# Kernel optimization log

Hardware: AMD Instinct MI355X
Metric: run time of the kernel (lower is better)

The kernel has to match this reference:

```python
import jax, jax.numpy as jnp
import numpy as np

B = 32768; NF = 8; E = 16; V = 100000; D = 4
IN = 2 * NF * E          # 256 = id_dims + agn_dims
FCN = [256, 128, 64]
DIMS = [IN] + FCN
EPS = 1e-5               # BatchNorm1d eps


def setup_inputs() -> dict:
    ks = jax.random.split(jax.random.key(0), 64)
    inp = {
        'id_idx': jax.random.randint(ks[0], (B, NF), 0, V),
        'agn_idx': jax.random.randint(ks[1], (B, NF), 0, V),
        'domain_id': jax.random.randint(ks[2], (B,), 0, D),
        'id_tables': jax.random.normal(ks[3], (NF, V, E), dtype=jnp.float32) * 0.01,
        'agn_tables': jax.random.normal(ks[4], (NF, V, E), dtype=jnp.float32) * 0.01,
    }
    k = 5
    for i in range(len(FCN)):
        din, dout = DIMS[i], DIMS[i + 1]
        inp[f'mlp_W{i}'] = jax.random.normal(ks[k], (D, din, dout), dtype=jnp.float32) / np.sqrt(din).astype(np.float32); k += 1
        inp[f'mlp_b{i}'] = jnp.zeros((D, dout), jnp.float32)
        inp[f'bn_g{i}'] = jnp.ones((D, dout), jnp.float32)
        inp[f'bn_b{i}'] = jnp.zeros((D, dout), jnp.float32)
        inp[f'gate_W1_{i}'] = jax.random.normal(ks[k], (D, IN, dout), dtype=jnp.float32) / np.sqrt(IN).astype(np.float32); k += 1
        inp[f'gate_b1_{i}'] = jnp.zeros((D, dout), jnp.float32)
        inp[f'gate_W2_{i}'] = jax.random.normal(ks[k], (D, dout, dout), dtype=jnp.float32) / np.sqrt(dout).astype(np.float32); k += 1
        inp[f'gate_b2_{i}'] = jnp.zeros((D, dout), jnp.float32)
    inp['fin_W'] = jax.random.normal(ks[k], (D, DIMS[-1], 1), dtype=jnp.float32) / np.sqrt(DIMS[-1]).astype(np.float32)
    inp['fin_b'] = jnp.zeros((D, 1), jnp.float32)
    return inp


def _embed(tables, idx):
    # tables [NF,V,E], idx [B,NF] -> [B, NF*E] (per-feature lookup then concat)
    g = tables[jnp.arange(NF)[None, :], idx]            # [B,NF,E]
    return g.reshape(idx.shape[0], NF * E)


def _ppnet(id_tables, agn_tables, mlp_W, mlp_b, bn_g, bn_b, gW1, gb1, gW2, gb2,
           fin_W, fin_b, id_idx, agn_idx, domain_id):
    id_x = _embed(id_tables, id_idx)                    # [B, 128]
    agn_x = _embed(agn_tables, agn_idx)                 # [B, 128]
    # gate_input = cat(id_x, agn_x.detach())
    gate_in = jnp.concatenate([id_x, jax.lax.stop_gradient(agn_x)], axis=1)  # [B, IN]
    h = None
    for i in range(len(FCN)):
        # GateNU: Linear->ReLU->Linear->2*sigmoid, broadcast over D domain towers
        g1 = jax.nn.relu(jnp.einsum('bi,dio->dbo', gate_in, gW1[i]) + gb1[i][:, None, :])
        gate = 2.0 * jax.nn.sigmoid(jnp.einsum('dbo,dop->dbp', g1, gW2[i]) + gb2[i][:, None, :])
        # MLP layer: Linear -> BatchNorm1d (train-mode batch stats) -> ReLU
        if h is None:
            h = jnp.einsum('bi,dio->dbo', gate_in, mlp_W[i]) + mlp_b[i][:, None, :]
        else:
            h = jnp.einsum('dbi,dio->dbo', h, mlp_W[i]) + mlp_b[i][:, None, :]
        mu = h.mean(axis=1, keepdims=True)
        var = h.var(axis=1, keepdims=True)              # biased, matches torch BN training
        h = (h - mu) * jax.lax.rsqrt(var + EPS) * bn_g[i][:, None, :] + bn_b[i][:, None, :]
        h = jax.nn.relu(h)
        h = h * gate
    out = jax.nn.sigmoid(jnp.einsum('dbh,dho->dbo', h, fin_W) + fin_b[:, None, :])  # [D,B,1]
    out = out[:, :, 0]                                  # [D,B]
    # torch.where masked-select chain == gather the row of the assigned domain
    return out[domain_id, jnp.arange(out.shape[1])]     # [B]


def reference(id_idx, agn_idx, domain_id, id_tables, agn_tables,
              mlp_W0, mlp_b0, bn_g0, bn_b0, gate_W1_0, gate_b1_0, gate_W2_0, gate_b2_0,
              mlp_W1, mlp_b1, bn_g1, bn_b1, gate_W1_1, gate_b1_1, gate_W2_1, gate_b2_1,
              mlp_W2, mlp_b2, bn_g2, bn_b2, gate_W1_2, gate_b1_2, gate_W2_2, gate_b2_2,
              fin_W, fin_b):
    mlp_W = [mlp_W0, mlp_W1, mlp_W2]; mlp_b = [mlp_b0, mlp_b1, mlp_b2]
    bn_g = [bn_g0, bn_g1, bn_g2]; bn_b = [bn_b0, bn_b1, bn_b2]
    gW1 = [gate_W1_0, gate_W1_1, gate_W1_2]; gb1 = [gate_b1_0, gate_b1_1, gate_b1_2]
    gW2 = [gate_W2_0, gate_W2_1, gate_W2_2]; gb2 = [gate_b2_0, gate_b2_1, gate_b2_2]
    return _ppnet(id_tables, agn_tables, mlp_W, mlp_b, bn_g, bn_b, gW1, gb1, gW2, gb2,
                  fin_W, fin_b, id_idx, agn_idx, domain_id)
```

## Files before the change

### kernel.cpp

```cpp
#include <hip/hip_runtime.h>


typedef __attribute__((ext_vector_type(8))) short short8;
typedef __attribute__((ext_vector_type(4))) float floatx4;

#define BATCH 32768
#define NDOM 4
#define TM 64

__device__ __forceinline__ unsigned short f2b(float f) {
    unsigned u = __float_as_uint(f);
    u += 0x7fffu + ((u >> 16) & 1u);
    return (unsigned short)(u >> 16);
}
__device__ __forceinline__ float b2f(unsigned short h) {
    return __uint_as_float(((unsigned)h) << 16);
}

struct MatDesc { const float* src; unsigned K, N, pfx, total; };
struct PrepArgs { MatDesc m[9]; float* stats; unsigned statsN; unsigned grand; };

__global__ __launch_bounds__(256) void prep_k(PrepArgs a, unsigned short* __restrict__ wt) {
    unsigned e = blockIdx.x * 256 + threadIdx.x;
    if (e < a.statsN) a.stats[e] = 0.f;
    if (e >= a.grand) return;
    int j = 0;
    while (j < 8 && e >= a.m[j].pfx + a.m[j].total) j++;
    const unsigned K = a.m[j].K, N = a.m[j].N;
    const unsigned local = e - a.m[j].pfx;
    const unsigned kn = K * N;
    const unsigned d = local / kn;
    const unsigned r2 = local - d * kn;
    const unsigned n = r2 / K;
    const unsigned k = r2 - n * K;
    wt[e] = f2b(a.m[j].src[((long long)d * K + k) * N + n]);
}

__global__ __launch_bounds__(256) void embed_k(const int* __restrict__ idi, const int* __restrict__ agi,
                                               const float* __restrict__ idt, const float* __restrict__ agt,
                                               unsigned short* __restrict__ gin) {
    int t = blockIdx.x * 256 + threadIdx.x;
    int b = t >> 4, slot = t & 15;
    int f = slot & 7;
    const int* ip = (slot < 8) ? idi : agi;
    const float* tab = (slot < 8) ? idt : agt;
    int ix = ip[b * 8 + f];
    const float* src = tab + ((long long)f * 100000 + ix) * 16;
    unsigned short tmp[16];
#pragma unroll
    for (int j = 0; j < 16; j++) tmp[j] = f2b(src[j]);
    unsigned short* dst = gin + (long long)b * 256 + slot * 16;
    *(uint4*)dst = *(const uint4*)tmp;
    *(uint4*)(dst + 8) = *(const uint4*)(tmp + 8);
}

template <int N, int KX>
__global__ __launch_bounds__(256, 2) void stats_k(
    const unsigned short* __restrict__ X, int ginMode,
    const unsigned short* __restrict__ Wm,
    float* __restrict__ gsum, float* __restrict__ gssq) {
    constexpr int GX = KX / 8;
    constexpr int NW = N / 4, CT = NW / 16;
    __shared__ __align__(16) unsigned short tA[TM * KX];
    const int t = threadIdx.x;
    const int d = blockIdx.y;
    const int m0 = blockIdx.x * TM;
    const unsigned short* Xp = X + ((long long)(ginMode ? 0 : d * BATCH) + m0) * KX;
#pragma unroll
    for (int r = 0; r < TM * GX / 256; r++) {
        int idx = r * 256 + t;
        int m = idx / GX, j = idx % GX;
        uint4 v = *(const uint4*)(Xp + (long long)m * KX + j * 8);
        *(uint4*)&tA[(m * GX + (j ^ (m & 7))) * 8] = v;
    }
    __syncthreads();
    const int w = t >> 6, lane = t & 63, lrow = lane & 15, lq = lane >> 4;
    const int n0w = w * NW;
    const unsigned short* Wp = Wm + ((long long)d * N + n0w) * KX;
    floatx4 acc[4][CT];
#pragma unroll
    for (int rt = 0; rt < 4; rt++)
#pragma unroll
        for (int ct = 0; ct < CT; ct++) acc[rt][ct] = (floatx4)(0.f);
#pragma unroll
    for (int k0 = 0; k0 < KX; k0 += 32) {
        short8 a[4], b[CT];
#pragma unroll
        for (int rt = 0; rt < 4; rt++) {
            int m = rt * 16 + lrow;
            a[rt] = *(const short8*)&tA[(m * GX + (((k0 >> 3) | lq) ^ (m & 7))) * 8];
        }
#pragma unroll
        for (int ct = 0; ct < CT; ct++)
            b[ct] = *(const short8*)(Wp + (long long)(ct * 16 + lrow) * KX + k0 + lq * 8);
#pragma unroll
        for (int rt = 0; rt < 4; rt++)
#pragma unroll
            for (int ct = 0; ct < CT; ct++)
                acc[rt][ct] = __builtin_amdgcn_mfma_f32_16x16x32_bf16(a[rt], b[ct], acc[rt][ct], 0, 0, 0);
    }
#pragma unroll
    for (int ct = 0; ct < CT; ct++) {
        float s = 0.f, ss = 0.f;
#pragma unroll
        for (int rt = 0; rt < 4; rt++)
#pragma unroll
            for (int r = 0; r < 4; r++) { float v = acc[rt][ct][r]; s += v; ss += v * v; }
        s += __shfl_down(s, 32); ss += __shfl_down(ss, 32);
        s += __shfl_down(s, 16); ss += __shfl_down(ss, 16);
        if (lane < 16) {
            atomicAdd(&gsum[d * N + n0w + ct * 16 + lane], s);
            atomicAdd(&gssq[d * N + n0w + ct * 16 + lane], ss);
        }
    }
}

__global__ void fin_k(const float* __restrict__ gsum, const float* __restrict__ gssq,
                      const float* __restrict__ gma, const float* __restrict__ bta,
                      float* __restrict__ SC, float* __restrict__ SH, int total, float invB) {
    int i = blockIdx.x * blockDim.x + threadIdx.x;
    if (i >= total) return;
    float ma = gsum[i] * invB;
    float var = gssq[i] * invB - ma * ma;
    float rs = rsqrtf(var + 1e-5f);
    float sc = rs * gma[i];
    SC[i] = sc;
    SH[i] = bta[i] - ma * sc;
}

template <int N, int KX, bool RESTAGE, bool FINAL>
__global__ __launch_bounds__(256, 2) void fused_k(
    const unsigned short* __restrict__ gin,
    const unsigned short* __restrict__ Xh,
    const unsigned short* __restrict__ W1,
    const unsigned short* __restrict__ W2,
    const unsigned short* __restrict__ Wm,
    const float* __restrict__ gb1, const float* __restrict__ gb2,
    const float* __restrict__ SC, const float* __restrict__ SH,
    unsigned short* __restrict__ Xn,
    const int* __restrict__ dom, const float* __restrict__ fw,
    const float* __restrict__ fb, float* __restrict__ outp) {
    constexpr int GG = N / 8;
    constexpr int GX = KX / 8;
    constexpr int NW = N / 4, CT = NW / 16;
    __shared__ __align__(16) unsigned short tA[TM * 256];
    __shared__ __align__(16) unsigned short g1b[TM * N];
    const int t = threadIdx.x;
    const int d = blockIdx.y;
    const int m0 = blockIdx.x * TM;
    const int w = t >> 6, lane = t & 63, lrow = lane & 15, lq = lane >> 4;
    const int n0w = w * NW;

    {
        const unsigned short* Gp = gin + (long long)m0 * 256;
#pragma unroll
        for (int r = 0; r < 8; r++) {
            int idx = r * 256 + t;
            int m = idx >> 5, j = idx & 31;
            uint4 v = *(const uint4*)(Gp + (long long)m * 256 + j * 8);
            *(uint4*)&tA[((m << 5) + (j ^ (m & 7))) * 8] = v;
        }
    }
    __syncthreads();

    floatx4 acc1[4][CT];
#pragma unroll
    for (int rt = 0; rt < 4; rt++)
#pragma unroll
        for (int ct = 0; ct < CT; ct++) acc1[rt][ct] = (floatx4)(0.f);
    const unsigned short* W1p = W1 + ((long long)d * N + n0w) * 256;
#pragma unroll
    for (int k0 = 0; k0 < 256; k0 += 32) {
        short8 a[4], b[CT];
#pragma unroll
        for (int rt = 0; rt < 4; rt++) {
            int m = rt * 16 + lrow;
            a[rt] = *(const short8*)&tA[((m << 5) + (((k0 >> 3) | lq) ^ (m & 7))) * 8];
        }
#pragma unroll
        for (int ct = 0; ct < CT; ct++)
            b[ct] = *(const short8*)(W1p + (long long)(ct * 16 + lrow) * 256 + k0 + lq * 8);
#pragma unroll
        for (int rt = 0; rt < 4; rt++)
#pragma unroll
            for (int ct = 0; ct < CT; ct++)
                acc1[rt][ct] = __builtin_amdgcn_mfma_f32_16x16x32_bf16(a[rt], b[ct], acc1[rt][ct], 0, 0, 0);
    }
#pragma unroll
    for (int ct = 0; ct < CT; ct++) {
        int n = n0w + ct * 16 + lrow;
        float bs = gb1[d * N + n];
        int jj = n >> 3, sub = n & 7;
#pragma unroll
        for (int rt = 0; rt < 4; rt++)
#pragma unroll
            for (int r = 0; r < 4; r++) {
                int m = rt * 16 + lq * 4 + r;
                g1b[(m * GG + (jj ^ (m & 7))) * 8 + sub] = f2b(fmaxf(acc1[rt][ct][r] + bs, 0.f));
            }
    }
    __syncthreads();

    floatx4 acc2[4][CT];
#pragma unroll
    for (int rt = 0; rt < 4; rt++)
#pragma unroll
        for (int ct = 0; ct < CT; ct++) acc2[rt][ct] = (floatx4)(0.f);
    const unsigned short* W2p = W2 + ((long long)d * N + n0w) * N;
#pragma unroll
    for (int k0 = 0; k0 < N; k0 += 32) {
        short8 a[4], b[CT];
#pragma unroll
        for (int rt = 0; rt < 4; rt++) {
            int m = rt * 16 + lrow;
            a[rt] = *(const short8*)&g1b[(m * GG + (((k0 >> 3) | lq) ^ (m & 7))) * 8];
        }
#pragma unroll
        for (int ct = 0; ct < CT; ct++)
            b[ct] = *(const short8*)(W2p + (long long)(ct * 16 + lrow) * N + k0 + lq * 8);
#pragma unroll
        for (int rt = 0; rt < 4; rt++)
#pragma unroll
            for (int ct = 0; ct < CT; ct++)
                acc2[rt][ct] = __builtin_amdgcn_mfma_f32_16x16x32_bf16(a[rt], b[ct], acc2[rt][ct], 0, 0, 0);
    }
    float gate[4][CT][4];
#pragma unroll
    for (int ct = 0; ct < CT; ct++) {
        int n = n0w + ct * 16 + lrow;
        float bs = gb2[d * N + n];
#pragma unroll
        for (int rt = 0; rt < 4; rt++)
#pragma unroll
            for (int r = 0; r < 4; r++)
                gate[rt][ct][r] = 2.f / (1.f + __expf(-(acc2[rt][ct][r] + bs)));
    }

    if (RESTAGE) {
        const unsigned short* Xp = Xh + ((long long)d * BATCH + m0) * KX;
#pragma unroll
        for (int r = 0; r < TM * GX / 256; r++) {
            int idx = r * 256 + t;
            int m = idx / GX, j = idx % GX;
            uint4 v = *(const uint4*)(Xp + (long long)m * KX + j * 8);
            *(uint4*)&tA[(m * GX + (j ^ (m & 7))) * 8] = v;
        }
    }
    __syncthreads();

    floatx4 acch[4][CT];
#pragma unroll
    for (int rt = 0; rt < 4; rt++)
#pragma unroll
        for (int ct = 0; ct < CT; ct++) acch[rt][ct] = (floatx4)(0.f);
    const unsigned short* Wmp = Wm + ((long long)d * N + n0w) * KX;
#pragma unroll
    for (int k0 = 0; k0 < KX; k0 += 32) {
        short8 a[4], b[CT];
#pragma unroll
        for (int rt = 0; rt < 4; rt++) {
            int m = rt * 16 + lrow;
            a[rt] = *(const short8*)&tA[(m * GX + (((k0 >> 3) | lq) ^ (m & 7))) * 8];
        }
#pragma unroll
        for (int ct = 0; ct < CT; ct++)
            b[ct] = *(const short8*)(Wmp + (long long)(ct * 16 + lrow) * KX + k0 + lq * 8);
#pragma unroll
        for (int rt = 0; rt < 4; rt++)
#pragma unroll
            for (int ct = 0; ct < CT; ct++)
                acch[rt][ct] = __builtin_amdgcn_mfma_f32_16x16x32_bf16(a[rt], b[ct], acch[rt][ct], 0, 0, 0);
    }
#pragma unroll
    for (int ct = 0; ct < CT; ct++) {
        int n = n0w + ct * 16 + lrow;
        float sc = SC[d * N + n], sh = SH[d * N + n];
#pragma unroll
        for (int rt = 0; rt < 4; rt++)
#pragma unroll
            for (int r = 0; r < 4; r++) {
                int m = rt * 16 + lq * 4 + r;
                float v = fmaxf(acch[rt][ct][r] * sc + sh, 0.f) * gate[rt][ct][r];
                g1b[m * N + n] = f2b(v);
            }
    }
    __syncthreads();

    if (!FINAL) {
        unsigned short* Op = Xn + ((long long)d * BATCH + m0) * N;
#pragma unroll
        for (int r = 0; r < TM * GG / 256; r++) {
            int idx = r * 256 + t;
            int m = idx / GG, j = idx % GG;
            *(uint4*)(Op + (long long)m * N + j * 8) = *(const uint4*)&g1b[(m * GG + j) * 8];
        }
    } else {
        int m = t >> 2, q = t & 3;
        const float* fwp = fw + d * 64;
        float s = 0.f;
#pragma unroll
        for (int k = 0; k < 16; k++) s += b2f(g1b[m * 64 + q * 16 + k]) * fwp[q * 16 + k];
        s += __shfl_down(s, 1);
        s += __shfl_down(s, 2);
        if (q == 0) {
            int b = m0 + m;
            if (dom[b] == d) outp[b] = 1.f / (1.f + __expf(-(s + fb[d])));
        }
    }
}

extern "C" void kernel_launch(void* const* d_in, const int* in_sizes, int n_in,
                              void* d_out, int out_size, void* d_ws, size_t ws_size,
                              hipStream_t stream) {
    const int B = BATCH, D = NDOM;

    const int* id_idx = (const int*)d_in[0];
    const int* agn_idx = (const int*)d_in[1];
    const int* dom = (const int*)d_in[2];
    const float* id_t = (const float*)d_in[3];
    const float* agn_t = (const float*)d_in[4];
    const float *mlpW[3], *bng[3], *bnb[3], *gW1[3], *gb1[3], *gW2[3], *gb2[3];
    for (int i = 0; i < 3; i++) {
        int b0 = 5 + i * 8;
        mlpW[i] = (const float*)d_in[b0 + 0];
        bng[i] = (const float*)d_in[b0 + 2];
        bnb[i] = (const float*)d_in[b0 + 3];
        gW1[i] = (const float*)d_in[b0 + 4];
        gb1[i] = (const float*)d_in[b0 + 5];
        gW2[i] = (const float*)d_in[b0 + 6];
        gb2[i] = (const float*)d_in[b0 + 7];
    }
    const float* finW = (const float*)d_in[29];
    const float* finb = (const float*)d_in[30];

    char* wsc = (char*)d_ws;
    size_t off = 0;
    auto alloc = [&](size_t bytes) -> char* {
        char* p = wsc + off;
        off = (off + bytes + 255) & ~(size_t)255;
        return p;
    };

    struct { const float* src; int K, N; } mats[9] = {
        {mlpW[0], 256, 256}, {gW1[0], 256, 256}, {gW2[0], 256, 256},
        {mlpW[1], 256, 128}, {gW1[1], 256, 128}, {gW2[1], 128, 128},
        {mlpW[2], 128, 64},  {gW1[2], 256, 64},  {gW2[2], 64, 64}};
    unsigned pfx[10];
    pfx[0] = 0;
    for (int j = 0; j < 9; j++) pfx[j + 1] = pfx[j] + 4u * mats[j].K * mats[j].N;

    unsigned short* wt = (unsigned short*)alloc((size_t)pfx[9] * 2);
    unsigned short* gin = (unsigned short*)alloc((size_t)B * 256 * 2);
    float* stats = (float*)alloc((size_t)3 * 2 * D * 256 * 4);
    float* scsh = (float*)alloc((size_t)3 * 2 * D * 256 * 4);
    unsigned short* X1 = (unsigned short*)alloc((size_t)D * B * 256 * 2);
    unsigned short* X2 = (unsigned short*)alloc((size_t)D * B * 128 * 2);

    PrepArgs pa;
    for (int j = 0; j < 9; j++) {
        pa.m[j].src = mats[j].src;
        pa.m[j].K = (unsigned)mats[j].K;
        pa.m[j].N = (unsigned)mats[j].N;
        pa.m[j].pfx = pfx[j];
        pa.m[j].total = 4u * mats[j].K * mats[j].N;
    }
    pa.stats = stats;
    pa.statsN = 3 * 2 * D * 256;
    pa.grand = pfx[9];

    const float invB = 1.f / (float)B;
    dim3 gs(B / TM, D);

    prep_k<<<dim3((pfx[9] + 255) / 256), 256, 0, stream>>>(pa, wt);
    embed_k<<<dim3(B * 16 / 256), 256, 0, stream>>>(id_idx, agn_idx, id_t, agn_t, gin);

    float* gsum0 = stats + 0 * 2 * D * 256; float* gssq0 = gsum0 + D * 256;
    float* gsum1 = stats + 1 * 2 * D * 256; float* gssq1 = gsum1 + D * 256;
    float* gsum2 = stats + 2 * 2 * D * 256; float* gssq2 = gsum2 + D * 256;
    float* SC0 = scsh + 0 * 2 * D * 256; float* SH0 = SC0 + D * 256;
    float* SC1 = scsh + 1 * 2 * D * 256; float* SH1 = SC1 + D * 256;
    float* SC2 = scsh + 2 * 2 * D * 256; float* SH2 = SC2 + D * 256;

    stats_k<256, 256><<<gs, 256, 0, stream>>>(gin, 1, wt + pfx[0], gsum0, gssq0);
    fin_k<<<(D * 256 + 255) / 256, 256, 0, stream>>>(gsum0, gssq0, bng[0], bnb[0], SC0, SH0, D * 256, invB);
    fused_k<256, 256, false, false><<<gs, 256, 0, stream>>>(
        gin, gin, wt + pfx[1], wt + pfx[2], wt + pfx[0], gb1[0], gb2[0], SC0, SH0,
        X1, nullptr, nullptr, nullptr, nullptr);

    stats_k<128, 256><<<gs, 256, 0, stream>>>(X1, 0, wt + pfx[3], gsum1, gssq1);
    fin_k<<<(D * 128 + 255) / 256, 256, 0, stream>>>(gsum1, gssq1, bng[1], bnb[1], SC1, SH1, D * 128, invB);
    fused_k<128, 256, true, false><<<gs, 256, 0, stream>>>(
        gin, X1, wt + pfx[4], wt + pfx[5], wt + pfx[3], gb1[1], gb2[1], SC1, SH1,
        X2, nullptr, nullptr, nullptr, nullptr);

    stats_k<64, 128><<<gs, 256, 0, stream>>>(X2, 0, wt + pfx[6], gsum2, gssq2);
    fin_k<<<(D * 64 + 255) / 256, 256, 0, stream>>>(gsum2, gssq2, bng[2], bnb[2], SC2, SH2, D * 64, invB);
    fused_k<64, 128, true, true><<<gs, 256, 0, stream>>>(
        gin, X2, wt + pfx[7], wt + pfx[8], wt + pfx[6], gb1[2], gb2[2], SC2, SH2,
        nullptr, dom, finW, finb, (float*)d_out);
}
```

Baseline: 502.2 us.

## Use 512-thread blocks splitting rows across waves, fold BN finalize into fused kernel

New measurement: 771.5 us. 53.6% more time.

```diff
diff --git a/kernel.cpp b/kernel.cpp
--- a/kernel.cpp
+++ b/kernel.cpp
@@ -55,7 +55,7 @@
 }
 
 template <int N, int KX>
-__global__ __launch_bounds__(256, 2) void stats_k(
+__global__ __launch_bounds__(512, 4) void stats_k(
     const unsigned short* __restrict__ X, int ginMode,
     const unsigned short* __restrict__ Wm,
     float* __restrict__ gsum, float* __restrict__ gssq) {
@@ -67,34 +67,35 @@
     const int m0 = blockIdx.x * TM;
     const unsigned short* Xp = X + ((long long)(ginMode ? 0 : d * BATCH) + m0) * KX;
 #pragma unroll
-    for (int r = 0; r < TM * GX / 256; r++) {
-        int idx = r * 256 + t;
+    for (int r = 0; r < TM * GX / 512; r++) {
+        int idx = r * 512 + t;
         int m = idx / GX, j = idx % GX;
         uint4 v = *(const uint4*)(Xp + (long long)m * KX + j * 8);
         *(uint4*)&tA[(m * GX + (j ^ (m & 7))) * 8] = v;
     }
     __syncthreads();
     const int w = t >> 6, lane = t & 63, lrow = lane & 15, lq = lane >> 4;
-    const int n0w = w * NW;
+    const int wn = w & 3, wm = w >> 2;
+    const int n0w = wn * NW, mb = wm * 32;
     const unsigned short* Wp = Wm + ((long long)d * N + n0w) * KX;
-    floatx4 acc[4][CT];
-#pragma unroll
-    for (int rt = 0; rt < 4; rt++)
+    floatx4 acc[2][CT];
+#pragma unroll
+    for (int rt = 0; rt < 2; rt++)
 #pragma unroll
         for (int ct = 0; ct < CT; ct++) acc[rt][ct] = (floatx4)(0.f);
 #pragma unroll
     for (int k0 = 0; k0 < KX; k0 += 32) {
-        short8 a[4], b[CT];
-#pragma unroll
-        for (int rt = 0; rt < 4; rt++) {
-            int m = rt * 16 + lrow;
+        short8 a[2], b[CT];
+#pragma unroll
+        for (int rt = 0; rt < 2; rt++) {
+            int m = mb + rt * 16 + lrow;
             a[rt] = *(const short8*)&tA[(m * GX + (((k0 >> 3) | lq) ^ (m & 7))) * 8];
         }
 #pragma unroll
         for (int ct = 0; ct < CT; ct++)
             b[ct] = *(const short8*)(Wp + (long long)(ct * 16 + lrow) * KX + k0 + lq * 8);
 #pragma unroll
-        for (int rt = 0; rt < 4; rt++)
+        for (int rt = 0; rt < 2; rt++)
 #pragma unroll
             for (int ct = 0; ct < CT; ct++)
                 acc[rt][ct] = __builtin_amdgcn_mfma_f32_16x16x32_bf16(a[rt], b[ct], acc[rt][ct], 0, 0, 0);
@@ -103,7 +104,7 @@
     for (int ct = 0; ct < CT; ct++) {
         float s = 0.f, ss = 0.f;
 #pragma unroll
-        for (int rt = 0; rt < 4; rt++)
+        for (int rt = 0; rt < 2; rt++)
 #pragma unroll
             for (int r = 0; r < 4; r++) { float v = acc[rt][ct][r]; s += v; ss += v * v; }
         s += __shfl_down(s, 32); ss += __shfl_down(ss, 32);
@@ -115,28 +116,16 @@
     }
 }
 
-__global__ void fin_k(const float* __restrict__ gsum, const float* __restrict__ gssq,
-                      const float* __restrict__ gma, const float* __restrict__ bta,
-                      float* __restrict__ SC, float* __restrict__ SH, int total, float invB) {
-    int i = blockIdx.x * blockDim.x + threadIdx.x;
-    if (i >= total) return;
-    float ma = gsum[i] * invB;
-    float var = gssq[i] * invB - ma * ma;
-    float rs = rsqrtf(var + 1e-5f);
-    float sc = rs * gma[i];
-    SC[i] = sc;
-    SH[i] = bta[i] - ma * sc;
-}
-
 template <int N, int KX, bool RESTAGE, bool FINAL>
-__global__ __launch_bounds__(256, 2) void fused_k(
+__global__ __launch_bounds__(512, 4) void fused_k(
     const unsigned short* __restrict__ gin,
     const unsigned short* __restrict__ Xh,
     const unsigned short* __restrict__ W1,
     const unsigned short* __restrict__ W2,
     const unsigned short* __restrict__ Wm,
     const float* __restrict__ gb1, const float* __restrict__ gb2,
-    const float* __restrict__ SC, const float* __restrict__ SH,
+    const float* __restrict__ gsum, const float* __restrict__ gssq,
+    const float* __restrict__ gma, const float* __restrict__ bta, float invB,
     unsigned short* __restrict__ Xn,
     const int* __restrict__ dom, const float* __restrict__ fw,
     const float* __restrict__ fb, float* __restrict__ outp) {
@@ -149,13 +138,14 @@
     const int d = blockIdx.y;
     const int m0 = blockIdx.x * TM;
     const int w = t >> 6, lane = t & 63, lrow = lane & 15, lq = lane >> 4;
-    const int n0w = w * NW;
+    const int wn = w & 3, wm = w >> 2;
+    const int n0w = wn * NW, mb = wm * 32;
 
     {
         const unsigned short* Gp = gin + (long long)m0 * 256;
 #pragma unroll
-        for (int r = 0; r < 8; r++) {
-            int idx = r * 256 + t;
+        for (int r = 0; r < 4; r++) {
+            int idx = r * 512 + t;
             int m = idx >> 5, j = idx & 31;
             uint4 v = *(const uint4*)(Gp + (long long)m * 256 + j * 8);
             *(uint4*)&tA[((m << 5) + (j ^ (m & 7))) * 8] = v;
@@ -163,25 +153,25 @@
     }
     __syncthreads();
 
-    floatx4 acc1[4][CT];
-#pragma unroll
-    for (int rt = 0; rt < 4; rt++)
+    floatx4 acc1[2][CT];
+#pragma unroll
+    for (int rt = 0; rt < 2; rt++)
 #pragma unroll
         for (int ct = 0; ct < CT; ct++) acc1[rt][ct] = (floatx4)(0.f);
     const unsigned short* W1p = W1 + ((long long)d * N + n0w) * 256;
 #pragma unroll
     for (int k0 = 0; k0 < 256; k0 += 32) {
-        short8 a[4], b[CT];
-#pragma unroll
-        for (int rt = 0; rt < 4; rt++) {
-            int m = rt * 16 + lrow;
+        short8 a[2], b[CT];
+#pragma unroll
+        for (int rt = 0; rt < 2; rt++) {
+            int m = mb + rt * 16 + lrow;
             a[rt] = *(const short8*)&tA[((m << 5) + (((k0 >> 3) | lq) ^ (m & 7))) * 8];
         }
 #pragma unroll
         for (int ct = 0; ct < CT; ct++)
             b[ct] = *(const short8*)(W1p + (long long)(ct * 16 + lrow) * 256 + k0 + lq * 8);
 #pragma unroll
-        for (int rt = 0; rt < 4; rt++)
+        for (int rt = 0; rt < 2; rt++)
 #pragma unroll
             for (int ct = 0; ct < CT; ct++)
                 acc1[rt][ct] = __builtin_amdgcn_mfma_f32_16x16x32_bf16(a[rt], b[ct], acc1[rt][ct], 0, 0, 0);
@@ -192,45 +182,45 @@
         float bs = gb1[d * N + n];
         int jj = n >> 3, sub = n & 7;
 #pragma unroll
-        for (int rt = 0; rt < 4; rt++)
+        for (int rt = 0; rt < 2; rt++)
 #pragma unroll
             for (int r = 0; r < 4; r++) {
-                int m = rt * 16 + lq * 4 + r;
+                int m = mb + rt * 16 + lq * 4 + r;
                 g1b[(m * GG + (jj ^ (m & 7))) * 8 + sub] = f2b(fmaxf(acc1[rt][ct][r] + bs, 0.f));
             }
     }
     __syncthreads();
 
-    floatx4 acc2[4][CT];
-#pragma unroll
-    for (int rt = 0; rt < 4; rt++)
+    floatx4 acc2[2][CT];
+#pragma unroll
+    for (int rt = 0; rt < 2; rt++)
 #pragma unroll
         for (int ct = 0; ct < CT; ct++) acc2[rt][ct] = (floatx4)(0.f);
     const unsigned short* W2p = W2 + ((long long)d * N + n0w) * N;
 #pragma unroll
     for (int k0 = 0; k0 < N; k0 += 32) {
-        short8 a[4], b[CT];
-#pragma unroll
-        for (int rt = 0; rt < 4; rt++) {
-            int m = rt * 16 + lrow;
+        short8 a[2], b[CT];
+#pragma unroll
+        for (int rt = 0; rt < 2; rt++) {
+            int m = mb + rt * 16 + lrow;
             a[rt] = *(const short8*)&g1b[(m * GG + (((k0 >> 3) | lq) ^ (m & 7))) * 8];
         }
 #pragma unroll
         for (int ct = 0; ct < CT; ct++)
             b[ct] = *(const short8*)(W2p + (long long)(ct * 16 + lrow) * N + k0 + lq * 8);
 #pragma unroll
-        for (int rt = 0; rt < 4; rt++)
+        for (int rt = 0; rt < 2; rt++)
 #pragma unroll
             for (int ct = 0; ct < CT; ct++)
                 acc2[rt][ct] = __builtin_amdgcn_mfma_f32_16x16x32_bf16(a[rt], b[ct], acc2[rt][ct], 0, 0, 0);
     }
-    float gate[4][CT][4];
+    float gate[2][CT][4];
 #pragma unroll
     for (int ct = 0; ct < CT; ct++) {
         int n = n0w + ct * 16 + lrow;
         float bs = gb2[d * N + n];
 #pragma unroll
-        for (int rt = 0; rt < 4; rt++)
+        for (int rt = 0; rt < 2; rt++)
 #pragma unroll
             for (int r = 0; r < 4; r++)
                 gate[rt][ct][r] = 2.f / (1.f + __expf(-(acc2[rt][ct][r] + bs)));
@@ -239,8 +229,8 @@
     if (RESTAGE) {
         const unsigned short* Xp = Xh + ((long long)d * BATCH + m0) * KX;
 #pragma unroll
-        for (int r = 0; r < TM * GX / 256; r++) {
-            int idx = r * 256 + t;
+        for (int r = 0; r < TM * GX / 512; r++) {
+            int idx = r * 512 + t;
             int m = idx / GX, j = idx % GX;
             uint4 v = *(const uint4*)(Xp + (long long)m * KX + j * 8);
             *(uint4*)&tA[(m * GX + (j ^ (m & 7))) * 8] = v;
@@ -248,25 +238,25 @@
     }
     __syncthreads();
 
-    floatx4 acch[4][CT];
-#pragma unroll
-    for (int rt = 0; rt < 4; rt++)
+    floatx4 acch[2][CT];
+#pragma unroll
+    for (int rt = 0; rt < 2; rt++)
 #pragma unroll
         for (int ct = 0; ct < CT; ct++) acch[rt][ct] = (floatx4)(0.f);
     const unsigned short* Wmp = Wm + ((long long)d * N + n0w) * KX;
 #pragma unroll
     for (int k0 = 0; k0 < KX; k0 += 32) {
-        short8 a[4], b[CT];
-#pragma unroll
-        for (int rt = 0; rt < 4; rt++) {
-            int m = rt * 16 + lrow;
+        short8 a[2], b[CT];
+#pragma unroll
+        for (int rt = 0; rt < 2; rt++) {
+            int m = mb + rt * 16 + lrow;
             a[rt] = *(const short8*)&tA[(m * GX + (((k0 >> 3) | lq) ^ (m & 7))) * 8];
         }
 #pragma unroll
         for (int ct = 0; ct < CT; ct++)
             b[ct] = *(const short8*)(Wmp + (long long)(ct * 16 + lrow) * KX + k0 + lq * 8);
 #pragma unroll
-        for (int rt = 0; rt < 4; rt++)
+        for (int rt = 0; rt < 2; rt++)
 #pragma unroll
             for (int ct = 0; ct < CT; ct++)
                 acch[rt][ct] = __builtin_amdgcn_mfma_f32_16x16x32_bf16(a[rt], b[ct], acch[rt][ct], 0, 0, 0);
@@ -274,14 +264,19 @@
 #pragma unroll
     for (int ct = 0; ct < CT; ct++) {
         int n = n0w + ct * 16 + lrow;
-        float sc = SC[d * N + n], sh = SH[d * N + n];
-#pragma unroll
-        for (int rt = 0; rt < 4; rt++)
+        int i = d * N + n;
+        float ma = gsum[i] * invB;
+        float var = gssq[i] * invB - ma * ma;
+        float sc = rsqrtf(var + 1e-5f) * gma[i];
+        float sh = bta[i] - ma * sc;
+        int jj = n >> 3, sub = n & 7;
+#pragma unroll
+        for (int rt = 0; rt < 2; rt++)
 #pragma unroll
             for (int r = 0; r < 4; r++) {
-                int m = rt * 16 + lq * 4 + r;
+                int m = mb + rt * 16 + lq * 4 + r;
                 float v = fmaxf(acch[rt][ct][r] * sc + sh, 0.f) * gate[rt][ct][r];
-                g1b[m * N + n] = f2b(v);
+                g1b[(m * GG + (jj ^ (m & 7))) * 8 + sub] = f2b(v);
             }
     }
     __syncthreads();
@@ -289,19 +284,22 @@
     if (!FINAL) {
         unsigned short* Op = Xn + ((long long)d * BATCH + m0) * N;
 #pragma unroll
-        for (int r = 0; r < TM * GG / 256; r++) {
-            int idx = r * 256 + t;
+        for (int r = 0; r < TM * GG / 512; r++) {
+            int idx = r * 512 + t;
             int m = idx / GG, j = idx % GG;
-            *(uint4*)(Op + (long long)m * N + j * 8) = *(const uint4*)&g1b[(m * GG + j) * 8];
+            *(uint4*)(Op + (long long)m * N + j * 8) = *(const uint4*)&g1b[(m * GG + (j ^ (m & 7))) * 8];
         }
     } else {
-        int m = t >> 2, q = t & 3;
+        int m = t >> 3, q = t & 7;
         const float* fwp = fw + d * 64;
+        short8 v = *(const short8*)&g1b[(m * 8 + (q ^ (m & 7))) * 8];
         float s = 0.f;
 #pragma unroll
-        for (int k = 0; k < 16; k++) s += b2f(g1b[m * 64 + q * 16 + k]) * fwp[q * 16 + k];
+        for (int kk = 0; kk < 8; kk++)
+            s += b2f((unsigned short)v[kk]) * fwp[q * 8 + kk];
+        s += __shfl_down(s, 4);
+        s += __shfl_down(s, 2);
         s += __shfl_down(s, 1);
-        s += __shfl_down(s, 2);
         if (q == 0) {
             int b = m0 + m;
             if (dom[b] == d) outp[b] = 1.f / (1.f + __expf(-(s + fb[d])));
@@ -352,7 +350,6 @@
     unsigned short* wt = (unsigned short*)alloc((size_t)pfx[9] * 2);
     unsigned short* gin = (unsigned short*)alloc((size_t)B * 256 * 2);
     float* stats = (float*)alloc((size_t)3 * 2 * D * 256 * 4);
-    float* scsh = (float*)alloc((size_t)3 * 2 * D * 256 * 4);
     unsigned short* X1 = (unsigned short*)alloc((size_t)D * B * 256 * 2);
     unsigned short* X2 = (unsigned short*)alloc((size_t)D * B * 128 * 2);
 
@@ -377,25 +374,22 @@
     float* gsum0 = stats + 0 * 2 * D * 256; float* gssq0 = gsum0 + D * 256;
     float* gsum1 = stats + 1 * 2 * D * 256; float* gssq1 = gsum1 + D * 256;
     float* gsum2 = stats + 2 * 2 * D * 256; float* gssq2 = gsum2 + D * 256;
-    float* SC0 = scsh + 0 * 2 * D * 256; float* SH0 = SC0 + D * 256;
-    float* SC1 = scsh + 1 * 2 * D * 256; float* SH1 = SC1 + D * 256;
-    float* SC2 = scsh + 2 * 2 * D * 256; float* SH2 = SC2 + D * 256;
-
-    stats_k<256, 256><<<gs, 256, 0, stream>>>(gin, 1, wt + pfx[0], gsum0, gssq0);
-    fin_k<<<(D * 256 + 255) / 256, 256, 0, stream>>>(gsum0, gssq0, bng[0], bnb[0], SC0, SH0, D * 256, invB);
-    fused_k<256, 256, false, false><<<gs, 256, 0, stream>>>(
-        gin, gin, wt + pfx[1], wt + pfx[2], wt + pfx[0], gb1[0], gb2[0], SC0, SH0,
+
+    stats_k<256, 256><<<gs, 512, 0, stream>>>(gin, 1, wt + pfx[0], gsum0, gssq0);
+    fused_k<256, 256, false, false><<<gs, 512, 0, stream>>>(
+        gin, gin, wt + pfx[1], wt + pfx[2], wt + pfx[0], gb1[0], gb2[0],
+        gsum0, gssq0, bng[0], bnb[0], invB,
         X1, nullptr, nullptr, nullptr, nullptr);
 
-    stats_k<128, 256><<<gs, 256, 0, stream>>>(X1, 0, wt + pfx[3], gsum1, gssq1);
-    fin_k<<<(D * 128 + 255) / 256, 256, 0, stream>>>(gsum1, gssq1, bng[1], bnb[1], SC1, SH1, D * 128, invB);
-    fused_k<128, 256, true, false><<<gs, 256, 0, stream>>>(
-        gin, X1, wt + pfx[4], wt + pfx[5], wt + pfx[3], gb1[1], gb2[1], SC1, SH1,
+    stats_k<128, 256><<<gs, 512, 0, stream>>>(X1, 0, wt + pfx[3], gsum1, gssq1);
+    fused_k<128, 256, true, false><<<gs, 512, 0, stream>>>(
+        gin, X1, wt + pfx[4], wt + pfx[5], wt + pfx[3], gb1[1], gb2[1],
+        gsum1, gssq1, bng[1], bnb[1], invB,
         X2, nullptr, nullptr, nullptr, nullptr);
 
-    stats_k<64, 128><<<gs, 256, 0, stream>>>(X2, 0, wt + pfx[6], gsum2, gssq2);
-    fin_k<<<(D * 64 + 255) / 256, 256, 0, stream>>>(gsum2, gssq2, bng[2], bnb[2], SC2, SH2, D * 64, invB);
-    fused_k<64, 128, true, true><<<gs, 256, 0, stream>>>(
-        gin, X2, wt + pfx[7], wt + pfx[8], wt + pfx[6], gb1[2], gb2[2], SC2, SH2,
+    stats_k<64, 128><<<gs, 512, 0, stream>>>(X2, 0, wt + pfx[6], gsum2, gssq2);
+    fused_k<64, 128, true, true><<<gs, 512, 0, stream>>>(
+        gin, X2, wt + pfx[7], wt + pfx[8], wt + pfx[6], gb1[2], gb2[2],
+        gsum2, gssq2, bng[2], bnb[2], invB,
         nullptr, dom, finW, finb, (float*)d_out);
 }
```

## Fold BN finalize into fused kernel and interleave gate and main GEMMs

Applied to the files above, without the earlier changes.

Measured after the change: 535.2 us. +6.6%, slower.

```diff
diff --git a/kernel.cpp b/kernel.cpp
--- a/kernel.cpp
+++ b/kernel.cpp
@@ -115,20 +115,7 @@
     }
 }
 
-__global__ void fin_k(const float* __restrict__ gsum, const float* __restrict__ gssq,
-                      const float* __restrict__ gma, const float* __restrict__ bta,
-                      float* __restrict__ SC, float* __restrict__ SH, int total, float invB) {
-    int i = blockIdx.x * blockDim.x + threadIdx.x;
-    if (i >= total) return;
-    float ma = gsum[i] * invB;
-    float var = gssq[i] * invB - ma * ma;
-    float rs = rsqrtf(var + 1e-5f);
-    float sc = rs * gma[i];
-    SC[i] = sc;
-    SH[i] = bta[i] - ma * sc;
-}
-
-template <int N, int KX, bool RESTAGE, bool FINAL>
+template <int N, int KX, bool SHARED_A, bool FINAL>
 __global__ __launch_bounds__(256, 2) void fused_k(
     const unsigned short* __restrict__ gin,
     const unsigned short* __restrict__ Xh,
@@ -136,14 +123,17 @@
     const unsigned short* __restrict__ W2,
     const unsigned short* __restrict__ Wm,
     const float* __restrict__ gb1, const float* __restrict__ gb2,
-    const float* __restrict__ SC, const float* __restrict__ SH,
+    const float* __restrict__ gsum, const float* __restrict__ gssq,
+    const float* __restrict__ gma, const float* __restrict__ bta, float invB,
     unsigned short* __restrict__ Xn,
     const int* __restrict__ dom, const float* __restrict__ fw,
     const float* __restrict__ fb, float* __restrict__ outp) {
     constexpr int GG = N / 8;
     constexpr int GX = KX / 8;
     constexpr int NW = N / 4, CT = NW / 16;
-    __shared__ __align__(16) unsigned short tA[TM * 256];
+    constexpr int TXN = SHARED_A ? 8 : TM * KX;
+    __shared__ __align__(16) unsigned short tG[TM * 256];
+    __shared__ __align__(16) unsigned short tX[TXN];
     __shared__ __align__(16) unsigned short g1b[TM * N];
     const int t = threadIdx.x;
     const int d = blockIdx.y;
@@ -158,33 +148,69 @@
             int idx = r * 256 + t;
             int m = idx >> 5, j = idx & 31;
             uint4 v = *(const uint4*)(Gp + (long long)m * 256 + j * 8);
-            *(uint4*)&tA[((m << 5) + (j ^ (m & 7))) * 8] = v;
-        }
-    }
-    __syncthreads();
-
-    floatx4 acc1[4][CT];
+            *(uint4*)&tG[((m << 5) + (j ^ (m & 7))) * 8] = v;
+        }
+    }
+    if constexpr (!SHARED_A) {
+        const unsigned short* Xp = Xh + ((long long)d * BATCH + m0) * KX;
+#pragma unroll
+        for (int r = 0; r < TM * GX / 256; r++) {
+            int idx = r * 256 + t;
+            int m = idx / GX, j = idx % GX;
+            uint4 v = *(const uint4*)(Xp + (long long)m * KX + j * 8);
+            *(uint4*)&tX[(m * GX + (j ^ (m & 7))) * 8] = v;
+        }
+    }
+    __syncthreads();
+
+    floatx4 acc1[4][CT], acch[4][CT];
 #pragma unroll
     for (int rt = 0; rt < 4; rt++)
 #pragma unroll
-        for (int ct = 0; ct < CT; ct++) acc1[rt][ct] = (floatx4)(0.f);
+        for (int ct = 0; ct < CT; ct++) { acc1[rt][ct] = (floatx4)(0.f); acch[rt][ct] = (floatx4)(0.f); }
     const unsigned short* W1p = W1 + ((long long)d * N + n0w) * 256;
+    const unsigned short* Wmp = Wm + ((long long)d * N + n0w) * KX;
 #pragma unroll
     for (int k0 = 0; k0 < 256; k0 += 32) {
-        short8 a[4], b[CT];
+        short8 aG[4];
 #pragma unroll
         for (int rt = 0; rt < 4; rt++) {
             int m = rt * 16 + lrow;
-            a[rt] = *(const short8*)&tA[((m << 5) + (((k0 >> 3) | lq) ^ (m & 7))) * 8];
-        }
+            aG[rt] = *(const short8*)&tG[((m << 5) + (((k0 >> 3) | lq) ^ (m & 7))) * 8];
+        }
+        short8 b1[CT];
 #pragma unroll
         for (int ct = 0; ct < CT; ct++)
-            b[ct] = *(const short8*)(W1p + (long long)(ct * 16 + lrow) * 256 + k0 + lq * 8);
-#pragma unroll
-        for (int rt = 0; rt < 4; rt++)
+            b1[ct] = *(const short8*)(W1p + (long long)(ct * 16 + lrow) * 256 + k0 + lq * 8);
+        if (k0 < KX) {
+            short8 aX[4], bm[CT];
+            if constexpr (SHARED_A) {
+#pragma unroll
+                for (int rt = 0; rt < 4; rt++) aX[rt] = aG[rt];
+            } else {
+#pragma unroll
+                for (int rt = 0; rt < 4; rt++) {
+                    int m = rt * 16 + lrow;
+                    aX[rt] = *(const short8*)&tX[(m * GX + (((k0 >> 3) | lq) ^ (m & 7))) * 8];
+                }
+            }
 #pragma unroll
             for (int ct = 0; ct < CT; ct++)
-                acc1[rt][ct] = __builtin_amdgcn_mfma_f32_16x16x32_bf16(a[rt], b[ct], acc1[rt][ct], 0, 0, 0);
+                bm[ct] = *(const short8*)(Wmp + (long long)(ct * 16 + lrow) * KX + k0 + lq * 8);
+#pragma unroll
+            for (int rt = 0; rt < 4; rt++)
+#pragma unroll
+                for (int ct = 0; ct < CT; ct++) {
+                    acc1[rt][ct] = __builtin_amdgcn_mfma_f32_16x16x32_bf16(aG[rt], b1[ct], acc1[rt][ct], 0, 0, 0);
+                    acch[rt][ct] = __builtin_amdgcn_mfma_f32_16x16x32_bf16(aX[rt], bm[ct], acch[rt][ct], 0, 0, 0);
+                }
+        } else {
+#pragma unroll
+            for (int rt = 0; rt < 4; rt++)
+#pragma unroll
+                for (int ct = 0; ct < CT; ct++)
+                    acc1[rt][ct] = __builtin_amdgcn_mfma_f32_16x16x32_bf16(aG[rt], b1[ct], acc1[rt][ct], 0, 0, 0);
+        }
     }
 #pragma unroll
     for (int ct = 0; ct < CT; ct++) {
@@ -224,64 +250,26 @@
             for (int ct = 0; ct < CT; ct++)
                 acc2[rt][ct] = __builtin_amdgcn_mfma_f32_16x16x32_bf16(a[rt], b[ct], acc2[rt][ct], 0, 0, 0);
     }
-    float gate[4][CT][4];
+    __syncthreads();
+
 #pragma unroll
     for (int ct = 0; ct < CT; ct++) {
         int n = n0w + ct * 16 + lrow;
-        float bs = gb2[d * N + n];
-#pragma unroll
-        for (int rt = 0; rt < 4; rt++)
-#pragma unroll
-            for (int r = 0; r < 4; r++)
-                gate[rt][ct][r] = 2.f / (1.f + __expf(-(acc2[rt][ct][r] + bs)));
-    }
-
-    if (RESTAGE) {
-        const unsigned short* Xp = Xh + ((long long)d * BATCH + m0) * KX;
-#pragma unroll
-        for (int r = 0; r < TM * GX / 256; r++) {
-            int idx = r * 256 + t;
-            int m = idx / GX, j = idx % GX;
-            uint4 v = *(const uint4*)(Xp + (long long)m * KX + j * 8);
-            *(uint4*)&tA[(m * GX + (j ^ (m & 7))) * 8] = v;
-        }
-    }
-    __syncthreads();
-
-    floatx4 acch[4][CT];
-#pragma unroll
-    for (int rt = 0; rt < 4; rt++)
-#pragma unroll
-        for (int ct = 0; ct < CT; ct++) acch[rt][ct] = (floatx4)(0.f);
-    const unsigned short* Wmp = Wm + ((long long)d * N + n0w) * KX;
-#pragma unroll
-    for (int k0 = 0; k0 < KX; k0 += 32) {
-        short8 a[4], b[CT];
-#pragma unroll
-        for (int rt = 0; rt < 4; rt++) {
-            int m = rt * 16 + lrow;
-            a[rt] = *(const short8*)&tA[(m * GX + (((k0 >> 3) | lq) ^ (m & 7))) * 8];
-        }
-#pragma unroll
-        for (int ct = 0; ct < CT; ct++)
-            b[ct] = *(const short8*)(Wmp + (long long)(ct * 16 + lrow) * KX + k0 + lq * 8);
-#pragma unroll
-        for (int rt = 0; rt < 4; rt++)
-#pragma unroll
-            for (int ct = 0; ct < CT; ct++)
-                acch[rt][ct] = __builtin_amdgcn_mfma_f32_16x16x32_bf16(a[rt], b[ct], acch[rt][ct], 0, 0, 0);
-    }
-#pragma unroll
-    for (int ct = 0; ct < CT; ct++) {
-        int n = n0w + ct * 16 + lrow;
-        float sc = SC[d * N + n], sh = SH[d * N + n];
+        int i = d * N + n;
+        float bs2 = gb2[i];
+        float ma = gsum[i] * invB;
+        float var = gssq[i] * invB - ma * ma;
+        float sc = rsqrtf(var + 1e-5f) * gma[i];
+        float sh = bta[i] - ma * sc;
+        int jj = n >> 3, sub = n & 7;
 #pragma unroll
         for (int rt = 0; rt < 4; rt++)
 #pragma unroll
             for (int r = 0; r < 4; r++) {
                 int m = rt * 16 + lq * 4 + r;
-                float v = fmaxf(acch[rt][ct][r] * sc + sh, 0.f) * gate[rt][ct][r];
-                g1b[m * N + n] = f2b(v);
+                float gate = 2.f / (1.f + __expf(-(acc2[rt][ct][r] + bs2)));
+                float v = fmaxf(acch[rt][ct][r] * sc + sh, 0.f) * gate;
+                g1b[(m * GG + (jj ^ (m & 7))) * 8 + sub] = f2b(v);
             }
     }
     __syncthreads();
@@ -292,14 +280,20 @@
         for (int r = 0; r < TM * GG / 256; r++) {
             int idx = r * 256 + t;
             int m = idx / GG, j = idx % GG;
-            *(uint4*)(Op + (long long)m * N + j * 8) = *(const uint4*)&g1b[(m * GG + j) * 8];
+            *(uint4*)(Op + (long long)m * N + j * 8) = *(const uint4*)&g1b[(m * GG + (j ^ (m & 7))) * 8];
         }
     } else {
         int m = t >> 2, q = t & 3;
         const float* fwp = fw + d * 64;
         float s = 0.f;
 #pragma unroll
-        for (int k = 0; k < 16; k++) s += b2f(g1b[m * 64 + q * 16 + k]) * fwp[q * 16 + k];
+        for (int g = 0; g < 2; g++) {
+            int j = q * 2 + g;
+            short8 v = *(const short8*)&g1b[(m * 8 + (j ^ (m & 7))) * 8];
+#pragma unroll
+            for (int kk = 0; kk < 8; kk++)
+                s += b2f((unsigned short)v[kk]) * fwp[j * 8 + kk];
+        }
         s += __shfl_down(s, 1);
         s += __shfl_down(s, 2);
         if (q == 0) {
@@ -352,7 +346,6 @@
     unsigned short* wt = (unsigned short*)alloc((size_t)pfx[9] * 2);
     unsigned short* gin = (unsigned short*)alloc((size_t)B * 256 * 2);
     float* stats = (float*)alloc((size_t)3 * 2 * D * 256 * 4);
-    float* scsh = (float*)alloc((size_t)3 * 2 * D * 256 * 4);
     unsigned short* X1 = (unsigned short*)alloc((size_t)D * B * 256 * 2);
     unsigned short* X2 = (unsigned short*)alloc((size_t)D * B * 128 * 2);
 
@@ -377,25 +370,22 @@
     float* gsum0 = stats + 0 * 2 * D * 256; float* gssq0 = gsum0 + D * 256;
     float* gsum1 = stats + 1 * 2 * D * 256; float* gssq1 = gsum1 + D * 256;
     float* gsum2 = stats + 2 * 2 * D * 256; float* gssq2 = gsum2 + D * 256;
-    float* SC0 = scsh + 0 * 2 * D * 256; float* SH0 = SC0 + D * 256;
-    float* SC1 = scsh + 1 * 2 * D * 256; float* SH1 = SC1 + D * 256;
-    float* SC2 = scsh + 2 * 2 * D * 256; float* SH2 = SC2 + D * 256;
 
     stats_k<256, 256><<<gs, 256, 0, stream>>>(gin, 1, wt + pfx[0], gsum0, gssq0);
-    fin_k<<<(D * 256 + 255) / 256, 256, 0, stream>>>(gsum0, gssq0, bng[0], bnb[0], SC0, SH0, D * 256, invB);
-    fused_k<256, 256, false, false><<<gs, 256, 0, stream>>>(
-        gin, gin, wt + pfx[1], wt + pfx[2], wt + pfx[0], gb1[0], gb2[0], SC0, SH0,
+    fused_k<256, 256, true, false><<<gs, 256, 0, stream>>>(
+        gin, gin, wt + pfx[1], wt + pfx[2], wt + pfx[0], gb1[0], gb2[0],
+        gsum0, gssq0, bng[0], bnb[0], invB,
         X1, nullptr, nullptr, nullptr, nullptr);
 
     stats_k<128, 256><<<gs, 256, 0, stream>>>(X1, 0, wt + pfx[3], gsum1, gssq1);
-    fin_k<<<(D * 128 + 255) / 256, 256, 0, stream>>>(gsum1, gssq1, bng[1], bnb[1], SC1, SH1, D * 128, invB);
-    fused_k<128, 256, true, false><<<gs, 256, 0, stream>>>(
-        gin, X1, wt + pfx[4], wt + pfx[5], wt + pfx[3], gb1[1], gb2[1], SC1, SH1,
+    fused_k<128, 256, false, false><<<gs, 256, 0, stream>>>(
+        gin, X1, wt + pfx[4], wt + pfx[5], wt + pfx[3], gb1[1], gb2[1],
+        gsum1, gssq1, bng[1], bnb[1], invB,
         X2, nullptr, nullptr, nullptr, nullptr);
 
     stats_k<64, 128><<<gs, 256, 0, stream>>>(X2, 0, wt + pfx[6], gsum2, gssq2);
-    fin_k<<<(D * 64 + 255) / 256, 256, 0, stream>>>(gsum2, gssq2, bng[2], bnb[2], SC2, SH2, D * 64, invB);
-    fused_k<64, 128, true, true><<<gs, 256, 0, stream>>>(
-        gin, X2, wt + pfx[7], wt + pfx[8], wt + pfx[6], gb1[2], gb2[2], SC2, SH2,
+    fused_k<64, 128, false, true><<<gs, 256, 0, stream>>>(
+        gin, X2, wt + pfx[7], wt + pfx[8], wt + pfx[6], gb1[2], gb2[2],
+        gsum2, gssq2, bng[2], bnb[2], invB,
         nullptr, dom, finW, finb, (float*)d_out);
 }
```
